# Performance work log

Measured on AMD Instinct MI355X. Metric: run time of the kernel, lower is better.

## Reference

```python
import jax, jax.numpy as jnp
import numpy as np

B, C, M, N = 16, 512, 256, 4096

def setup_inputs() -> dict:
    key = jax.random.key(0)
    k1, k2, k3 = jax.random.split(key, 3)
    x = jax.random.normal(k1, (B, C, N), dtype=jnp.float32)
    # Conv1d(C, M, 1, bias=False) weight: [M, C] (kernel size 1 squeezed)
    Wk = jax.random.normal(k2, (M, C), dtype=jnp.float32) * (1.0 / np.sqrt(C))
    # Conv1d(M, C, 1, bias=False) weight: [C, M]
    Wv = jax.random.normal(k3, (C, M), dtype=jnp.float32) * (1.0 / np.sqrt(M))
    return {"x": x, "Wk": Wk, "Wv": Wv}

def reference(x, Wk, Wv):
    # attn = M_k(x): 1x1 conv == matmul over channel dim -> [B, M, N]
    attn = jnp.einsum("mc,bcn->bmn", Wk, x)
    # softmax over sequence dim N
    attn = jax.nn.softmax(attn, axis=2)
    # L1 normalization over memory-unit (channel) dim M
    attn = attn / (1e-9 + attn.sum(axis=1, keepdims=True))
    # out = M_v(attn): [B, C, N]
    out = jnp.einsum("cm,bmn->bcn", Wv, attn)
    return x + out
```

## Files before the change

kernel.cpp:

```cpp
#include <hip/hip_runtime.h>
#include <hip/hip_bf16.h>

#define Bdim 16
#define Cdim 512
#define Mdim 256
#define Ndim 4096

typedef short bf16x8 __attribute__((ext_vector_type(8)));
typedef float f32x4 __attribute__((ext_vector_type(4)));
typedef unsigned short us8 __attribute__((ext_vector_type(8)));
typedef unsigned short us4 __attribute__((ext_vector_type(4)));

__device__ __forceinline__ unsigned short f2b(float f) {
  union { float f; unsigned int u; } v; v.f = f;
  return (unsigned short)((v.u + 0x8000u) >> 16);
}
__device__ __forceinline__ float b2f(unsigned short h) {
  union { unsigned int u; float f; } v; v.u = ((unsigned int)h) << 16;
  return v.f;
}

#define K1_PAD 72

__global__ __launch_bounds__(256) void k1_gemm1(
    const float* __restrict__ gx, const float* __restrict__ gWk,
    unsigned short* __restrict__ gS) {
  __shared__ unsigned short Wk_s[128 * K1_PAD];
  __shared__ unsigned short xT_s[128 * K1_PAD];
  const int t = threadIdx.x;
  const int b = blockIdx.z;
  const int m0 = blockIdx.y * 128;
  const int n0 = blockIdx.x * 128;
  const int w = t >> 6;
  const int lane = t & 63;
  const int lr = lane & 15;
  const int lg = lane >> 4;
  const int wm = (w >> 1) * 64;
  const int wn = (w & 1) * 64;

  f32x4 acc[4][4] = {};
  const float* xb = gx + (size_t)b * Cdim * Ndim;

  for (int ck = 0; ck < Cdim; ck += 64) {
#pragma unroll
    for (int i = 0; i < 4; ++i) {
      int q = i * 256 + t;
      int r = q >> 3;
      int c8 = (q & 7) * 8;
      const float* src = gWk + (size_t)(m0 + r) * Cdim + ck + c8;
      f32x4 v0 = *reinterpret_cast<const f32x4*>(src);
      f32x4 v1 = *reinterpret_cast<const f32x4*>(src + 4);
      us8 h;
      h[0] = f2b(v0[0]); h[1] = f2b(v0[1]); h[2] = f2b(v0[2]); h[3] = f2b(v0[3]);
      h[4] = f2b(v1[0]); h[5] = f2b(v1[1]); h[6] = f2b(v1[2]); h[7] = f2b(v1[3]);
      *reinterpret_cast<us8*>(&Wk_s[r * K1_PAD + c8]) = h;
    }
    {
      const int nl = t & 63;
      const int cb = (t >> 6) * 16;
#pragma unroll
      for (int h = 0; h < 2; ++h) {
        const int n = nl + h * 64;
        const float* src = xb + (size_t)(ck + cb) * Ndim + n0 + n;
        float xv[16];
#pragma unroll
        for (int j = 0; j < 16; ++j) xv[j] = src[(size_t)j * Ndim];
        us8 h0, h1;
#pragma unroll
        for (int j = 0; j < 8; ++j) { h0[j] = f2b(xv[j]); h1[j] = f2b(xv[8 + j]); }
        *reinterpret_cast<us8*>(&xT_s[n * K1_PAD + cb]) = h0;
        *reinterpret_cast<us8*>(&xT_s[n * K1_PAD + cb + 8]) = h1;
      }
    }
    __syncthreads();
#pragma unroll
    for (int kk = 0; kk < 64; kk += 32) {
      bf16x8 af[4], bfr[4];
#pragma unroll
      for (int mi = 0; mi < 4; ++mi)
        af[mi] = *reinterpret_cast<const bf16x8*>(
            &Wk_s[(wm + mi * 16 + lr) * K1_PAD + kk + lg * 8]);
#pragma unroll
      for (int ni = 0; ni < 4; ++ni)
        bfr[ni] = *reinterpret_cast<const bf16x8*>(
            &xT_s[(wn + ni * 16 + lr) * K1_PAD + kk + lg * 8]);
#pragma unroll
      for (int mi = 0; mi < 4; ++mi)
#pragma unroll
        for (int ni = 0; ni < 4; ++ni)
          acc[mi][ni] = __builtin_amdgcn_mfma_f32_16x16x32_bf16(
              af[mi], bfr[ni], acc[mi][ni], 0, 0, 0);
    }
    __syncthreads();
  }
  unsigned short* Sb = gS + ((size_t)b * Mdim + m0 + wm) * Ndim + n0 + wn;
#pragma unroll
  for (int mi = 0; mi < 4; ++mi)
#pragma unroll
    for (int ni = 0; ni < 4; ++ni)
#pragma unroll
      for (int r = 0; r < 4; ++r) {
        int m = mi * 16 + lg * 4 + r;
        int n = ni * 16 + lr;
        Sb[(size_t)m * Ndim + n] = f2b(acc[mi][ni][r]);
      }
}

__global__ __launch_bounds__(256) void k2_rowstats(
    const unsigned short* __restrict__ gS, float2* __restrict__ stats) {
  const int m = blockIdx.x;
  const int b = blockIdx.y;
  const unsigned short* row = gS + ((size_t)b * Mdim + m) * Ndim;
  const int t = threadIdx.x;
  const int w = t >> 6;
  float v[16];
#pragma unroll
  for (int i = 0; i < 2; ++i) {
    us8 u = *reinterpret_cast<const us8*>(row + i * 2048 + t * 8);
#pragma unroll
    for (int j = 0; j < 8; ++j) v[i * 8 + j] = b2f(u[j]);
  }
  float mx = -1e30f;
#pragma unroll
  for (int i = 0; i < 16; ++i) mx = fmaxf(mx, v[i]);
#pragma unroll
  for (int o = 32; o > 0; o >>= 1) mx = fmaxf(mx, __shfl_xor(mx, o, 64));
  __shared__ float redmax[4], redsum[4];
  if ((t & 63) == 0) redmax[w] = mx;
  __syncthreads();
  mx = fmaxf(fmaxf(redmax[0], redmax[1]), fmaxf(redmax[2], redmax[3]));
  float s = 0.f;
#pragma unroll
  for (int i = 0; i < 16; ++i) s += __expf(v[i] - mx);
#pragma unroll
  for (int o = 32; o > 0; o >>= 1) s += __shfl_xor(s, o, 64);
  if ((t & 63) == 0) redsum[w] = s;
  __syncthreads();
  if (t == 0) {
    float tot = redsum[0] + redsum[1] + redsum[2] + redsum[3];
    stats[(size_t)b * Mdim + m] = make_float2(mx, 1.0f / tot);
  }
}

__global__ __launch_bounds__(256) void k3_norm(
    const unsigned short* __restrict__ gS, const float2* __restrict__ stats,
    unsigned short* __restrict__ gPT) {
  const int b = blockIdx.y;
  const int n0 = blockIdx.x * 64;
  __shared__ unsigned short P_s[256 * 66];
  __shared__ float cs[4][64];
  __shared__ float rtot[64];
  const int t = threadIdx.x;
  const int w = t >> 6;
  const int l = t & 63;
  float acc = 0.f;
  const unsigned short* Sb = gS + (size_t)b * Mdim * Ndim + n0;
#pragma unroll 4
  for (int i = 0; i < 64; ++i) {
    int m = i * 4 + w;
    float2 st = stats[b * Mdim + m];
    float p = __expf(b2f(Sb[(size_t)m * Ndim + l]) - st.x) * st.y;
    acc += p;
    P_s[m * 66 + l] = f2b(p);
  }
  cs[w][l] = acc;
  __syncthreads();
  if (w == 0) rtot[l] = 1.0f / (1e-9f + cs[0][l] + cs[1][l] + cs[2][l] + cs[3][l]);
  __syncthreads();
  const int n = t >> 2;
  const int mb = (t & 3) * 64;
  const float rc = rtot[n];
  unsigned short* dst = gPT + ((size_t)b * Ndim + n0 + n) * Mdim + mb;
#pragma unroll
  for (int j = 0; j < 64; j += 8) {
    us8 pk;
#pragma unroll
    for (int jj = 0; jj < 8; ++jj)
      pk[jj] = f2b(b2f(P_s[(mb + j + jj) * 66 + n]) * rc);
    *reinterpret_cast<us8*>(dst + j) = pk;
  }
}

#define K4_P 136

__global__ __launch_bounds__(256) void k4_gemm2(
    const float* __restrict__ gx, const float* __restrict__ gWv,
    const unsigned short* __restrict__ gPT, float* __restrict__ gout) {
  __shared__ unsigned short Wv_s[64 * K4_P];
  __shared__ unsigned short PT_s[64 * K4_P];
  const int t = threadIdx.x;
  const int b = blockIdx.z;
  const int c0 = blockIdx.y * 64;
  const int n0 = blockIdx.x * 64;
  const int w = t >> 6;
  const int lane = t & 63;
  const int lr = lane & 15;
  const int lg = lane >> 4;
  const int wc = (w >> 1) * 32;
  const int wn = (w & 1) * 32;

  f32x4 acc[2][2] = {};

  for (int ck = 0; ck < Mdim; ck += 128) {
#pragma unroll
    for (int i = 0; i < 8; ++i) {
      int q = i * 256 + t;
      int r = q >> 5;
      int mq = (q & 31) * 4;
      f32x4 v = *reinterpret_cast<const f32x4*>(gWv + (size_t)(c0 + r) * Mdim + ck + mq);
      us4 h;
      h[0] = f2b(v[0]); h[1] = f2b(v[1]); h[2] = f2b(v[2]); h[3] = f2b(v[3]);
      *reinterpret_cast<us4*>(&Wv_s[r * K4_P + mq]) = h;
    }
#pragma unroll
    for (int i = 0; i < 4; ++i) {
      int q = i * 256 + t;
      int r = q >> 4;
      int mq = (q & 15) * 8;
      us8 u = *reinterpret_cast<const us8*>(gPT + ((size_t)b * Ndim + n0 + r) * Mdim + ck + mq);
      *reinterpret_cast<us8*>(&PT_s[r * K4_P + mq]) = u;
    }
    __syncthreads();
#pragma unroll
    for (int kk = 0; kk < 128; kk += 32) {
      bf16x8 af[2], bfr[2];
#pragma unroll
      for (int ci = 0; ci < 2; ++ci)
        af[ci] = *reinterpret_cast<const bf16x8*>(
            &Wv_s[(wc + ci * 16 + lr) * K4_P + kk + lg * 8]);
#pragma unroll
      for (int ni = 0; ni < 2; ++ni)
        bfr[ni] = *reinterpret_cast<const bf16x8*>(
            &PT_s[(wn + ni * 16 + lr) * K4_P + kk + lg * 8]);
#pragma unroll
      for (int ci = 0; ci < 2; ++ci)
#pragma unroll
        for (int ni = 0; ni < 2; ++ni)
          acc[ci][ni] = __builtin_amdgcn_mfma_f32_16x16x32_bf16(
              af[ci], bfr[ni], acc[ci][ni], 0, 0, 0);
    }
    __syncthreads();
  }
#pragma unroll
  for (int ci = 0; ci < 2; ++ci)
#pragma unroll
    for (int ni = 0; ni < 2; ++ni)
#pragma unroll
      for (int r = 0; r < 4; ++r) {
        int c = c0 + wc + ci * 16 + lg * 4 + r;
        int n = n0 + wn + ni * 16 + lr;
        size_t idx = ((size_t)b * Cdim + c) * Ndim + n;
        gout[idx] = gx[idx] + acc[ci][ni][r];
      }
}

extern "C" void kernel_launch(void* const* d_in, const int* in_sizes, int n_in,
                              void* d_out, int out_size, void* d_ws, size_t ws_size,
                              hipStream_t stream) {
  const float* x = (const float*)d_in[0];
  const float* Wk = (const float*)d_in[1];
  const float* Wv = (const float*)d_in[2];
  float* out = (float*)d_out;

  unsigned short* S = (unsigned short*)d_ws;
  unsigned short* PT = S + (size_t)Bdim * Mdim * Ndim;
  float2* stats = (float2*)(PT + (size_t)Bdim * Ndim * Mdim);

  k1_gemm1<<<dim3(Ndim / 128, Mdim / 128, Bdim), 256, 0, stream>>>(x, Wk, S);
  k2_rowstats<<<dim3(Mdim, Bdim), 256, 0, stream>>>(S, stats);
  k3_norm<<<dim3(Ndim / 64, Bdim), 256, 0, stream>>>(S, stats, PT);
  k4_gemm2<<<dim3(Ndim / 64, Cdim / 64, Bdim), 256, 0, stream>>>(x, Wv, PT, out);
}
```

Measured before the change: 135.1 us.

## Pre-convert weights to bf16, enlarge tiles, swizzle LDS, vectorize norm transpose

```diff
diff --git a/kernel.cpp b/kernel.cpp
--- a/kernel.cpp
+++ b/kernel.cpp
@@ -20,13 +20,23 @@
   return v.f;
 }
 
-#define K1_PAD 72
+__global__ __launch_bounds__(256) void k0_convert(
+    const float* __restrict__ gWk, const float* __restrict__ gWv,
+    unsigned short* __restrict__ oWk, unsigned short* __restrict__ oWv) {
+  const int i = (blockIdx.x * 256 + threadIdx.x) * 4;
+  f32x4 a = *reinterpret_cast<const f32x4*>(gWk + i);
+  f32x4 b = *reinterpret_cast<const f32x4*>(gWv + i);
+  us4 ha, hb;
+#pragma unroll
+  for (int j = 0; j < 4; ++j) { ha[j] = f2b(a[j]); hb[j] = f2b(b[j]); }
+  *reinterpret_cast<us4*>(oWk + i) = ha;
+  *reinterpret_cast<us4*>(oWv + i) = hb;
+}
 
 __global__ __launch_bounds__(256) void k1_gemm1(
-    const float* __restrict__ gx, const float* __restrict__ gWk,
+    const float* __restrict__ gx, const unsigned short* __restrict__ gWkB,
     unsigned short* __restrict__ gS) {
-  __shared__ unsigned short Wk_s[128 * K1_PAD];
-  __shared__ unsigned short xT_s[128 * K1_PAD];
+  __shared__ unsigned short xT_s[128 * 128];
   const int t = threadIdx.x;
   const int b = blockIdx.z;
   const int m0 = blockIdx.y * 128;
@@ -39,51 +49,42 @@
   const int wn = (w & 1) * 64;
 
   f32x4 acc[4][4] = {};
-  const float* xb = gx + (size_t)b * Cdim * Ndim;
-
-  for (int ck = 0; ck < Cdim; ck += 64) {
-#pragma unroll
-    for (int i = 0; i < 4; ++i) {
-      int q = i * 256 + t;
-      int r = q >> 3;
-      int c8 = (q & 7) * 8;
-      const float* src = gWk + (size_t)(m0 + r) * Cdim + ck + c8;
-      f32x4 v0 = *reinterpret_cast<const f32x4*>(src);
-      f32x4 v1 = *reinterpret_cast<const f32x4*>(src + 4);
-      us8 h;
-      h[0] = f2b(v0[0]); h[1] = f2b(v0[1]); h[2] = f2b(v0[2]); h[3] = f2b(v0[3]);
-      h[4] = f2b(v1[0]); h[5] = f2b(v1[1]); h[6] = f2b(v1[2]); h[7] = f2b(v1[3]);
-      *reinterpret_cast<us8*>(&Wk_s[r * K1_PAD + c8]) = h;
-    }
-    {
-      const int nl = t & 63;
-      const int cb = (t >> 6) * 16;
-#pragma unroll
-      for (int h = 0; h < 2; ++h) {
-        const int n = nl + h * 64;
-        const float* src = xb + (size_t)(ck + cb) * Ndim + n0 + n;
-        float xv[16];
-#pragma unroll
-        for (int j = 0; j < 16; ++j) xv[j] = src[(size_t)j * Ndim];
-        us8 h0, h1;
-#pragma unroll
-        for (int j = 0; j < 8; ++j) { h0[j] = f2b(xv[j]); h1[j] = f2b(xv[8 + j]); }
-        *reinterpret_cast<us8*>(&xT_s[n * K1_PAD + cb]) = h0;
-        *reinterpret_cast<us8*>(&xT_s[n * K1_PAD + cb + 8]) = h1;
+  const float* xb = gx + (size_t)b * Cdim * Ndim + n0;
+  const unsigned short* WkRow = gWkB + (size_t)(m0 + wm + lr) * Cdim + lg * 8;
+
+  const int snl = t & 63;
+  const int scb = (t >> 6) * 32;
+
+  for (int ck = 0; ck < Cdim; ck += 128) {
+#pragma unroll
+    for (int h = 0; h < 2; ++h) {
+      const int n = snl + h * 64;
+      const float* src = xb + (size_t)(ck + scb) * Ndim + n;
+      char* dstrow = reinterpret_cast<char*>(xT_s) + n * 256;
+      const int sw = (n & 7) << 4;
+#pragma unroll
+      for (int j8 = 0; j8 < 4; ++j8) {
+        us8 hsh;
+#pragma unroll
+        for (int j = 0; j < 8; ++j)
+          hsh[j] = (unsigned short)(__float_as_uint(src[(size_t)(j8 * 8 + j) * Ndim]) >> 16);
+        *reinterpret_cast<us8*>(dstrow + (((scb + j8 * 8) * 2) ^ sw)) = hsh;
       }
     }
     __syncthreads();
 #pragma unroll
-    for (int kk = 0; kk < 64; kk += 32) {
+    for (int kk = 0; kk < 128; kk += 32) {
       bf16x8 af[4], bfr[4];
 #pragma unroll
       for (int mi = 0; mi < 4; ++mi)
-        af[mi] = *reinterpret_cast<const bf16x8*>(
-            &Wk_s[(wm + mi * 16 + lr) * K1_PAD + kk + lg * 8]);
-#pragma unroll
-      for (int ni = 0; ni < 4; ++ni)
+        af[mi] = *reinterpret_cast<const bf16x8*>(WkRow + (size_t)mi * 16 * Cdim + ck + kk);
+#pragma unroll
+      for (int ni = 0; ni < 4; ++ni) {
+        const int r = wn + ni * 16 + lr;
         bfr[ni] = *reinterpret_cast<const bf16x8*>(
-            &xT_s[(wn + ni * 16 + lr) * K1_PAD + kk + lg * 8]);
+            reinterpret_cast<const char*>(xT_s) +
+            ((r * 256 + (kk + lg * 8) * 2) ^ ((r & 7) << 4)));
+      }
 #pragma unroll
       for (int mi = 0; mi < 4; ++mi)
 #pragma unroll
@@ -142,114 +143,118 @@
   }
 }
 
+#define K3_PAD 264
+
 __global__ __launch_bounds__(256) void k3_norm(
     const unsigned short* __restrict__ gS, const float2* __restrict__ stats,
     unsigned short* __restrict__ gPT) {
+  __shared__ unsigned short P_s[64 * K3_PAD];
+  __shared__ float cs[4][64];
+  __shared__ float rtot[64];
   const int b = blockIdx.y;
   const int n0 = blockIdx.x * 64;
-  __shared__ unsigned short P_s[256 * 66];
-  __shared__ float cs[4][64];
-  __shared__ float rtot[64];
   const int t = threadIdx.x;
   const int w = t >> 6;
   const int l = t & 63;
+  const unsigned short* Sb = gS + ((size_t)b * Mdim + w * 64) * Ndim + n0 + l;
+  const float2* stb = stats + (size_t)b * Mdim + w * 64;
   float acc = 0.f;
-  const unsigned short* Sb = gS + (size_t)b * Mdim * Ndim + n0;
-#pragma unroll 4
-  for (int i = 0; i < 64; ++i) {
-    int m = i * 4 + w;
-    float2 st = stats[b * Mdim + m];
-    float p = __expf(b2f(Sb[(size_t)m * Ndim + l]) - st.x) * st.y;
-    acc += p;
-    P_s[m * 66 + l] = f2b(p);
+#pragma unroll
+  for (int i8 = 0; i8 < 8; ++i8) {
+    us8 pk;
+#pragma unroll
+    for (int jj = 0; jj < 8; ++jj) {
+      const int mi = i8 * 8 + jj;
+      float2 st = stb[mi];
+      float p = __expf(b2f(Sb[(size_t)mi * Ndim]) - st.x) * st.y;
+      acc += p;
+      pk[jj] = f2b(p);
+    }
+    *reinterpret_cast<us8*>(&P_s[l * K3_PAD + w * 64 + i8 * 8]) = pk;
   }
   cs[w][l] = acc;
   __syncthreads();
   if (w == 0) rtot[l] = 1.0f / (1e-9f + cs[0][l] + cs[1][l] + cs[2][l] + cs[3][l]);
   __syncthreads();
-  const int n = t >> 2;
-  const int mb = (t & 3) * 64;
-  const float rc = rtot[n];
-  unsigned short* dst = gPT + ((size_t)b * Ndim + n0 + n) * Mdim + mb;
-#pragma unroll
-  for (int j = 0; j < 64; j += 8) {
-    us8 pk;
-#pragma unroll
-    for (int jj = 0; jj < 8; ++jj)
-      pk[jj] = f2b(b2f(P_s[(mb + j + jj) * 66 + n]) * rc);
-    *reinterpret_cast<us8*>(dst + j) = pk;
-  }
-}
-
-#define K4_P 136
+  const int mo = (t & 31) * 8;
+#pragma unroll
+  for (int j = 0; j < 8; ++j) {
+    const int n = (t >> 5) + j * 8;
+    const float rc = rtot[n];
+    us8 pv = *reinterpret_cast<const us8*>(&P_s[n * K3_PAD + mo]);
+    us8 o;
+#pragma unroll
+    for (int q = 0; q < 8; ++q) o[q] = f2b(b2f(pv[q]) * rc);
+    *reinterpret_cast<us8*>(gPT + ((size_t)b * Ndim + n0 + n) * Mdim + mo) = o;
+  }
+}
 
 __global__ __launch_bounds__(256) void k4_gemm2(
-    const float* __restrict__ gx, const float* __restrict__ gWv,
+    const float* __restrict__ gx, const unsigned short* __restrict__ gWvB,
     const unsigned short* __restrict__ gPT, float* __restrict__ gout) {
-  __shared__ unsigned short Wv_s[64 * K4_P];
-  __shared__ unsigned short PT_s[64 * K4_P];
+  __shared__ unsigned short PT_s[2][128 * 128];
   const int t = threadIdx.x;
   const int b = blockIdx.z;
-  const int c0 = blockIdx.y * 64;
-  const int n0 = blockIdx.x * 64;
+  const int c0 = blockIdx.y * 128;
+  const int n0 = blockIdx.x * 128;
   const int w = t >> 6;
   const int lane = t & 63;
   const int lr = lane & 15;
   const int lg = lane >> 4;
-  const int wc = (w >> 1) * 32;
-  const int wn = (w & 1) * 32;
-
-  f32x4 acc[2][2] = {};
-
-  for (int ck = 0; ck < Mdim; ck += 128) {
-#pragma unroll
-    for (int i = 0; i < 8; ++i) {
-      int q = i * 256 + t;
-      int r = q >> 5;
-      int mq = (q & 31) * 4;
-      f32x4 v = *reinterpret_cast<const f32x4*>(gWv + (size_t)(c0 + r) * Mdim + ck + mq);
-      us4 h;
-      h[0] = f2b(v[0]); h[1] = f2b(v[1]); h[2] = f2b(v[2]); h[3] = f2b(v[3]);
-      *reinterpret_cast<us4*>(&Wv_s[r * K4_P + mq]) = h;
-    }
-#pragma unroll
-    for (int i = 0; i < 4; ++i) {
-      int q = i * 256 + t;
-      int r = q >> 4;
-      int mq = (q & 15) * 8;
-      us8 u = *reinterpret_cast<const us8*>(gPT + ((size_t)b * Ndim + n0 + r) * Mdim + ck + mq);
-      *reinterpret_cast<us8*>(&PT_s[r * K4_P + mq]) = u;
-    }
-    __syncthreads();
+  const int wc = (w >> 1) * 64;
+  const int wn = (w & 1) * 64;
+
+  f32x4 acc[4][4] = {};
+
+  {
+    const int mo16 = (t & 15) * 16;
+    const int r0 = t >> 4;
+#pragma unroll
+    for (int s = 0; s < 2; ++s) {
+      char* tile = reinterpret_cast<char*>(PT_s[s]);
+#pragma unroll
+      for (int j = 0; j < 8; ++j) {
+        const int n = r0 + j * 16;
+        us8 v = *reinterpret_cast<const us8*>(
+            reinterpret_cast<const char*>(gPT) +
+            ((size_t)b * Ndim + n0 + n) * (Mdim * 2) + s * 256 + mo16);
+        *reinterpret_cast<us8*>(tile + n * 256 + (mo16 ^ ((n & 7) << 4))) = v;
+      }
+    }
+  }
+  __syncthreads();
+#pragma unroll
+  for (int s = 0; s < 2; ++s) {
+    const unsigned short* WvRow = gWvB + (size_t)(c0 + wc + lr) * Mdim + s * 128 + lg * 8;
+    const char* tile = reinterpret_cast<const char*>(PT_s[s]);
 #pragma unroll
     for (int kk = 0; kk < 128; kk += 32) {
-      bf16x8 af[2], bfr[2];
-#pragma unroll
-      for (int ci = 0; ci < 2; ++ci)
-        af[ci] = *reinterpret_cast<const bf16x8*>(
-            &Wv_s[(wc + ci * 16 + lr) * K4_P + kk + lg * 8]);
-#pragma unroll
-      for (int ni = 0; ni < 2; ++ni)
+      bf16x8 af[4], bfr[4];
+#pragma unroll
+      for (int ci = 0; ci < 4; ++ci)
+        af[ci] = *reinterpret_cast<const bf16x8*>(WvRow + (size_t)ci * 16 * Mdim + kk);
+#pragma unroll
+      for (int ni = 0; ni < 4; ++ni) {
+        const int rn = wn + ni * 16 + lr;
         bfr[ni] = *reinterpret_cast<const bf16x8*>(
-            &PT_s[(wn + ni * 16 + lr) * K4_P + kk + lg * 8]);
-#pragma unroll
-      for (int ci = 0; ci < 2; ++ci)
-#pragma unroll
-        for (int ni = 0; ni < 2; ++ni)
+            tile + ((rn * 256 + (kk + lg * 8) * 2) ^ ((rn & 7) << 4)));
+      }
+#pragma unroll
+      for (int ci = 0; ci < 4; ++ci)
+#pragma unroll
+        for (int ni = 0; ni < 4; ++ni)
           acc[ci][ni] = __builtin_amdgcn_mfma_f32_16x16x32_bf16(
               af[ci], bfr[ni], acc[ci][ni], 0, 0, 0);
     }
-    __syncthreads();
-  }
-#pragma unroll
-  for (int ci = 0; ci < 2; ++ci)
-#pragma unroll
-    for (int ni = 0; ni < 2; ++ni)
+  }
+  const size_t base = ((size_t)b * Cdim + c0 + wc) * Ndim + n0 + wn;
+#pragma unroll
+  for (int ci = 0; ci < 4; ++ci)
+#pragma unroll
+    for (int ni = 0; ni < 4; ++ni)
 #pragma unroll
       for (int r = 0; r < 4; ++r) {
-        int c = c0 + wc + ci * 16 + lg * 4 + r;
-        int n = n0 + wn + ni * 16 + lr;
-        size_t idx = ((size_t)b * Cdim + c) * Ndim + n;
+        size_t idx = base + (size_t)(ci * 16 + lg * 4 + r) * Ndim + ni * 16 + lr;
         gout[idx] = gx[idx] + acc[ci][ni][r];
       }
 }
@@ -265,9 +270,12 @@
   unsigned short* S = (unsigned short*)d_ws;
   unsigned short* PT = S + (size_t)Bdim * Mdim * Ndim;
   float2* stats = (float2*)(PT + (size_t)Bdim * Ndim * Mdim);
-
-  k1_gemm1<<<dim3(Ndim / 128, Mdim / 128, Bdim), 256, 0, stream>>>(x, Wk, S);
+  unsigned short* WkB = (unsigned short*)(stats + Bdim * Mdim);
+  unsigned short* WvB = WkB + Mdim * Cdim;
+
+  k0_convert<<<dim3((Mdim * Cdim) / 1024), 256, 0, stream>>>(Wk, Wv, WkB, WvB);
+  k1_gemm1<<<dim3(Ndim / 128, Mdim / 128, Bdim), 256, 0, stream>>>(x, WkB, S);
   k2_rowstats<<<dim3(Mdim, Bdim), 256, 0, stream>>>(S, stats);
   k3_norm<<<dim3(Ndim / 64, Bdim), 256, 0, stream>>>(S, stats, PT);
-  k4_gemm2<<<dim3(Ndim / 64, Cdim / 64, Bdim), 256, 0, stream>>>(x, Wv, PT, out);
-}
+  k4_gemm2<<<dim3(Ndim / 128, Cdim / 128, Bdim), 256, 0, stream>>>(x, WvB, PT, out);
+}
```

Result: slower. 181.6 us (+34.4%).
